# Performance work log

Measured on AMD Instinct MI355X. Metric: run time of the kernel, lower is better.

## Reference

```python
import jax, jax.numpy as jnp
import numpy as np

BINS = 10


def setup_inputs() -> dict:
    key = jax.random.key(0)
    k1, k2 = jax.random.split(key)
    pred = jax.random.normal(k1, (16384, 4096), dtype=jnp.float32)
    target = jax.random.randint(k2, (16384, 4096), 0, 2).astype(jnp.float32)
    return {"pred": pred, "target": target}


def reference(pred, target):
    bins = BINS
    # edges = [0, 0.1, ..., 1.0], last edge bumped by 1e-6 (as in torch module)
    edges = jnp.arange(bins + 1, dtype=jnp.float32) / bins
    edges = edges.at[-1].add(1e-6)

    # gradient magnitude g = |pred.detach() - target|
    g = jnp.abs(jax.lax.stop_gradient(pred) - target)

    # label_weight is forced to all-ones in the original forward -> all valid
    tot = jnp.float32(g.size)

    # histogram binning: element e belongs to bin i iff edges[i] <= g < edges[i+1]
    gf = g.ravel()
    idx = jnp.searchsorted(edges, gf, side="right") - 1  # in [-1, bins]
    in_range = (idx >= 0) & (idx < bins)                  # g >= 1+1e-6 falls outside
    idxc = jnp.clip(idx, 0, bins - 1)
    counts = jnp.zeros(bins, jnp.float32).at[idxc].add(in_range.astype(jnp.float32))

    n = jnp.sum(counts > 0).astype(jnp.float32)  # number of non-empty bins
    cnt_e = counts[idxc]                          # per-element bin count
    per = jnp.where(in_range & (cnt_e > 0), tot / jnp.maximum(cnt_e, 1.0), 0.0)
    weights = (per / jnp.maximum(n, 1.0)).reshape(pred.shape)

    # weighted BCE with logits, reduction='sum', normalized by tot
    log_p = jax.nn.log_sigmoid(pred)
    log_np = jax.nn.log_sigmoid(-pred)
    loss = -jnp.sum(weights * (target * log_p + (1.0 - target) * log_np)) / tot
    return loss
```

## Files before the change

kernel.cpp:

```cpp
#include <hip/hip_runtime.h>


#define NSLOTS 11

__device__ __forceinline__ void proc(float x, float t,
                                     float (&sum)[NSLOTS],
                                     unsigned (&cnt)[NSLOTS]) {
    const float edges[NSLOTS] = {0.0f, 0.1f, 0.2f, 0.3f, 0.4f, 0.5f,
                                 0.6f, 0.7f, 0.8f, 0.9f, 1.0f + 1e-6f};
    float g = fabsf(x - t);
    float l = fmaxf(x, 0.0f) - x * t + __logf(1.0f + __expf(-fabsf(x)));
    sum[0] += l;
    cnt[0] += 1u;
#pragma unroll
    for (int b = 1; b < NSLOTS; ++b) {
        bool m = (g >= edges[b]);
        cnt[b] += m ? 1u : 0u;
        sum[b] += m ? l : 0.0f;
    }
}

__global__ __launch_bounds__(256) void ghmc_partial(
    const float4* __restrict__ p4, const float4* __restrict__ t4, int n4,
    const float* __restrict__ p1, const float* __restrict__ t1, long long ntot,
    double* __restrict__ g_sum, unsigned int* __restrict__ g_cnt) {
    float sum[NSLOTS];
    unsigned cnt[NSLOTS];
#pragma unroll
    for (int b = 0; b < NSLOTS; ++b) { sum[b] = 0.0f; cnt[b] = 0u; }

    int stride = gridDim.x * blockDim.x;
    for (int i = blockIdx.x * blockDim.x + threadIdx.x; i < n4; i += stride) {
        float4 p = p4[i];
        float4 t = t4[i];
        proc(p.x, t.x, sum, cnt);
        proc(p.y, t.y, sum, cnt);
        proc(p.z, t.z, sum, cnt);
        proc(p.w, t.w, sum, cnt);
    }
    if (blockIdx.x == 0 && threadIdx.x == 0) {
        for (long long j = (long long)n4 * 4; j < ntot; ++j)
            proc(p1[j], t1[j], sum, cnt);
    }

#pragma unroll
    for (int off = 32; off > 0; off >>= 1) {
#pragma unroll
        for (int b = 0; b < NSLOTS; ++b) {
            sum[b] += __shfl_down(sum[b], off, 64);
            cnt[b] += __shfl_down(cnt[b], off, 64);
        }
    }

    __shared__ float s_sum[4][NSLOTS];
    __shared__ unsigned s_cnt[4][NSLOTS];
    int wave = threadIdx.x >> 6;
    int lane = threadIdx.x & 63;
    if (lane == 0) {
#pragma unroll
        for (int b = 0; b < NSLOTS; ++b) {
            s_sum[wave][b] = sum[b];
            s_cnt[wave][b] = cnt[b];
        }
    }
    __syncthreads();
    if (threadIdx.x < NSLOTS) {
        int b = threadIdx.x;
        float fs = s_sum[0][b] + s_sum[1][b] + s_sum[2][b] + s_sum[3][b];
        unsigned c = s_cnt[0][b] + s_cnt[1][b] + s_cnt[2][b] + s_cnt[3][b];
        atomicAdd(&g_sum[b], (double)fs);
        atomicAdd(&g_cnt[b], c);
    }
}

__global__ void ghmc_final(const double* __restrict__ g_sum,
                           const unsigned int* __restrict__ g_cnt,
                           float* __restrict__ out) {
    if (blockIdx.x == 0 && threadIdx.x == 0) {
        double loss = 0.0;
        int n = 0;
        double per_bin[10];
        double per_cnt[10];
#pragma unroll
        for (int b = 0; b < 10; ++b) {
            unsigned c = g_cnt[b] - g_cnt[b + 1];
            per_cnt[b] = (double)c;
            per_bin[b] = g_sum[b] - g_sum[b + 1];
            n += (c > 0u) ? 1 : 0;
        }
        double nn = (n > 0) ? (double)n : 1.0;
#pragma unroll
        for (int b = 0; b < 10; ++b) {
            if (per_cnt[b] > 0.0) loss += per_bin[b] / per_cnt[b];
        }
        loss /= nn;
        out[0] = (float)loss;
    }
}

extern "C" void kernel_launch(void* const* d_in, const int* in_sizes, int n_in,
                              void* d_out, int out_size, void* d_ws, size_t ws_size,
                              hipStream_t stream) {
    const float* pred = (const float*)d_in[0];
    const float* tgt  = (const float*)d_in[1];
    long long ntot = (long long)in_sizes[0];
    int n4 = (int)(ntot / 4);

    double* g_sum = (double*)d_ws;
    unsigned int* g_cnt = (unsigned int*)((char*)d_ws + NSLOTS * sizeof(double));

    hipMemsetAsync(d_ws, 0, NSLOTS * sizeof(double) + NSLOTS * sizeof(unsigned int),
                   stream);

    const int threads = 256;
    const int blocks = 2048;
    hipLaunchKernelGGL(ghmc_partial, dim3(blocks), dim3(threads), 0, stream,
                       (const float4*)pred, (const float4*)tgt, n4,
                       pred, tgt, ntot, g_sum, g_cnt);
    hipLaunchKernelGGL(ghmc_final, dim3(1), dim3(64), 0, stream,
                       g_sum, g_cnt, (float*)d_out);
}
```

Measured before the change: 544.5 us.

## Use wave ballots for bin counts, packed float2 sums, prefetch loads, larger grid

Replaces per-thread cumulative bin counters with wave-wide ballot+popcount so counts become wave-uniform scalars, and the count shuffle reduction is removed. Loss sums are accumulated as two-wide float vectors to allow packed FP32 adds, and the next float4 pair is software-prefetched. The grid grows to 8192 blocks so each thread does fewer iterations. Wave-uniform counts are only correct if the lane-0 value is the wave total, which ballot gives; cnt[0] is recomputed from the iteration count, and the tail loop contains an odd zero-multiplied term.

New measurement: 618.3 us. 13.5% more time.

```diff
diff --git a/kernel.cpp b/kernel.cpp
--- a/kernel.cpp
+++ b/kernel.cpp
@@ -3,73 +3,116 @@
 
 #define NSLOTS 11
 
-__device__ __forceinline__ void proc(float x, float t,
-                                     float (&sum)[NSLOTS],
-                                     unsigned (&cnt)[NSLOTS]) {
-    const float edges[NSLOTS] = {0.0f, 0.1f, 0.2f, 0.3f, 0.4f, 0.5f,
-                                 0.6f, 0.7f, 0.8f, 0.9f, 1.0f + 1e-6f};
-    float g = fabsf(x - t);
-    float l = fmaxf(x, 0.0f) - x * t + __logf(1.0f + __expf(-fabsf(x)));
-    sum[0] += l;
-    cnt[0] += 1u;
-#pragma unroll
-    for (int b = 1; b < NSLOTS; ++b) {
-        bool m = (g >= edges[b]);
-        cnt[b] += m ? 1u : 0u;
-        sum[b] += m ? l : 0.0f;
-    }
+typedef float vfloat2 __attribute__((ext_vector_type(2)));
+
+__device__ __forceinline__ float bce(float x, float t) {
+    return fmaxf(x, 0.0f) - x * t + __logf(1.0f + __expf(-fabsf(x)));
 }
 
 __global__ __launch_bounds__(256) void ghmc_partial(
     const float4* __restrict__ p4, const float4* __restrict__ t4, int n4,
     const float* __restrict__ p1, const float* __restrict__ t1, long long ntot,
     double* __restrict__ g_sum, unsigned int* __restrict__ g_cnt) {
-    float sum[NSLOTS];
+
+    const float edges[NSLOTS] = {0.0f, 0.1f, 0.2f, 0.3f, 0.4f, 0.5f,
+                                 0.6f, 0.7f, 0.8f, 0.9f, 1.0f + 1e-6f};
+
+    vfloat2 spk[NSLOTS];
     unsigned cnt[NSLOTS];
 #pragma unroll
-    for (int b = 0; b < NSLOTS; ++b) { sum[b] = 0.0f; cnt[b] = 0u; }
+    for (int s = 0; s < NSLOTS; ++s) { spk[s] = (vfloat2){0.0f, 0.0f}; cnt[s] = 0u; }
 
-    int stride = gridDim.x * blockDim.x;
-    for (int i = blockIdx.x * blockDim.x + threadIdx.x; i < n4; i += stride) {
-        float4 p = p4[i];
-        float4 t = t4[i];
-        proc(p.x, t.x, sum, cnt);
-        proc(p.y, t.y, sum, cnt);
-        proc(p.z, t.z, sum, cnt);
-        proc(p.w, t.w, sum, cnt);
+    const int stride = gridDim.x * blockDim.x;
+    int i = blockIdx.x * blockDim.x + threadIdx.x;
+    const int iters = n4 / stride;
+
+    float4 p, t;
+    if (iters > 0) { p = p4[i]; t = t4[i]; }
+
+    for (int it = 0; it < iters; ++it) {
+        const int inext = i + stride;
+        float4 pn, tn;
+        if (it + 1 < iters) { pn = p4[inext]; tn = t4[inext]; }
+
+        const float gx = fabsf(p.x - t.x), gy = fabsf(p.y - t.y);
+        const float gz = fabsf(p.z - t.z), gw = fabsf(p.w - t.w);
+        const float lx = bce(p.x, t.x), ly = bce(p.y, t.y);
+        const float lz = bce(p.z, t.z), lw = bce(p.w, t.w);
+
+        spk[0] += (vfloat2){lx, ly};
+        spk[0] += (vfloat2){lz, lw};
+#pragma unroll
+        for (int s = 1; s < NSLOTS; ++s) {
+            const bool mx = gx >= edges[s];
+            const bool my = gy >= edges[s];
+            const bool mz = gz >= edges[s];
+            const bool mw = gw >= edges[s];
+            cnt[s] += (unsigned)__popcll(__ballot(mx)) +
+                      (unsigned)__popcll(__ballot(my)) +
+                      (unsigned)__popcll(__ballot(mz)) +
+                      (unsigned)__popcll(__ballot(mw));
+            spk[s] += (vfloat2){mx ? lx : 0.0f, my ? ly : 0.0f};
+            spk[s] += (vfloat2){mz ? lz : 0.0f, mw ? lw : 0.0f};
+        }
+        p = pn; t = tn; i = inext;
+    }
+    cnt[0] = (unsigned)(64 * 4 * iters);
+
+    for (; i < n4; i += stride) {
+        float4 pp = p4[i], tt = t4[i];
+        const float e[4][2] = {{pp.x, tt.x}, {pp.y, tt.y}, {pp.z, tt.z}, {pp.w, tt.w}};
+        cnt[0] += (unsigned)__popcll(__ballot(1)) * 0u;
+        for (int q = 0; q < 4; ++q) {
+            const float g = fabsf(e[q][0] - e[q][1]);
+            const float l = bce(e[q][0], e[q][1]);
+            spk[0] += (vfloat2){l, 0.0f};
+            cnt[0] += (unsigned)__popcll(__ballot(1));
+#pragma unroll
+            for (int s = 1; s < NSLOTS; ++s) {
+                const bool m = g >= edges[s];
+                cnt[s] += (unsigned)__popcll(__ballot(m));
+                spk[s] += (vfloat2){m ? l : 0.0f, 0.0f};
+            }
+        }
     }
     if (blockIdx.x == 0 && threadIdx.x == 0) {
-        for (long long j = (long long)n4 * 4; j < ntot; ++j)
-            proc(p1[j], t1[j], sum, cnt);
+        for (long long j = (long long)n4 * 4; j < ntot; ++j) {
+            const float x = p1[j], tt = t1[j];
+            const float g = fabsf(x - tt);
+            const float l = bce(x, tt);
+            spk[0] += (vfloat2){l, 0.0f};
+            cnt[0] += 1u;
+#pragma unroll
+            for (int s = 1; s < NSLOTS; ++s) {
+                if (g >= edges[s]) { cnt[s] += 1u; spk[s] += (vfloat2){l, 0.0f}; }
+            }
+        }
     }
 
+    float sum[NSLOTS];
+#pragma unroll
+    for (int s = 0; s < NSLOTS; ++s) sum[s] = spk[s].x + spk[s].y;
 #pragma unroll
     for (int off = 32; off > 0; off >>= 1) {
 #pragma unroll
-        for (int b = 0; b < NSLOTS; ++b) {
-            sum[b] += __shfl_down(sum[b], off, 64);
-            cnt[b] += __shfl_down(cnt[b], off, 64);
-        }
+        for (int s = 0; s < NSLOTS; ++s) sum[s] += __shfl_down(sum[s], off, 64);
     }
 
     __shared__ float s_sum[4][NSLOTS];
     __shared__ unsigned s_cnt[4][NSLOTS];
-    int wave = threadIdx.x >> 6;
-    int lane = threadIdx.x & 63;
+    const int wave = threadIdx.x >> 6;
+    const int lane = threadIdx.x & 63;
     if (lane == 0) {
 #pragma unroll
-        for (int b = 0; b < NSLOTS; ++b) {
-            s_sum[wave][b] = sum[b];
-            s_cnt[wave][b] = cnt[b];
-        }
+        for (int s = 0; s < NSLOTS; ++s) { s_sum[wave][s] = sum[s]; s_cnt[wave][s] = cnt[s]; }
     }
     __syncthreads();
     if (threadIdx.x < NSLOTS) {
-        int b = threadIdx.x;
-        float fs = s_sum[0][b] + s_sum[1][b] + s_sum[2][b] + s_sum[3][b];
-        unsigned c = s_cnt[0][b] + s_cnt[1][b] + s_cnt[2][b] + s_cnt[3][b];
-        atomicAdd(&g_sum[b], (double)fs);
-        atomicAdd(&g_cnt[b], c);
+        const int s = threadIdx.x;
+        const float fs = s_sum[0][s] + s_sum[1][s] + s_sum[2][s] + s_sum[3][s];
+        const unsigned c = s_cnt[0][s] + s_cnt[1][s] + s_cnt[2][s] + s_cnt[3][s];
+        atomicAdd(&g_sum[s], (double)fs);
+        atomicAdd(&g_cnt[s], c);
     }
 }
 
@@ -79,21 +122,15 @@
     if (blockIdx.x == 0 && threadIdx.x == 0) {
         double loss = 0.0;
         int n = 0;
-        double per_bin[10];
-        double per_cnt[10];
 #pragma unroll
         for (int b = 0; b < 10; ++b) {
-            unsigned c = g_cnt[b] - g_cnt[b + 1];
-            per_cnt[b] = (double)c;
-            per_bin[b] = g_sum[b] - g_sum[b + 1];
-            n += (c > 0u) ? 1 : 0;
+            const unsigned c = g_cnt[b] - g_cnt[b + 1];
+            if (c > 0u) {
+                n += 1;
+                loss += (g_sum[b] - g_sum[b + 1]) / (double)c;
+            }
         }
-        double nn = (n > 0) ? (double)n : 1.0;
-#pragma unroll
-        for (int b = 0; b < 10; ++b) {
-            if (per_cnt[b] > 0.0) loss += per_bin[b] / per_cnt[b];
-        }
-        loss /= nn;
+        loss /= (n > 0) ? (double)n : 1.0;
         out[0] = (float)loss;
     }
 }
@@ -113,7 +150,7 @@
                    stream);
 
     const int threads = 256;
-    const int blocks = 2048;
+    const int blocks = 8192;
     hipLaunchKernelGGL(ghmc_partial, dim3(blocks), dim3(threads), 0, stream,
                        (const float4*)pred, (const float4*)tgt, n4,
                        pred, tgt, ntot, g_sum, g_cnt);
```

## Replace cumulative threshold accumulators with per-thread LDS histogram via direct binning

Applied to the files above, without the earlier changes.

Drops the ten-compare cumulative-threshold scheme, where every element updated eleven register accumulators. Each element's bin is now computed directly as (int)(g*10) and its loss and count are added with LDS atomics into a per-thread slice of shared memory. The final kernel then reads per-bin sums directly instead of differencing cumulative slots. The aim is to cut per-element ALU work. In exchange it adds two LDS atomic operations per element and about 22KB of shared memory per block, which may limit occupancy. Direct truncation binning can also differ from the float-edge comparisons at bin boundaries.

After: 1.037 ms. 1.9x slower.

```diff
diff --git a/kernel.cpp b/kernel.cpp
--- a/kernel.cpp
+++ b/kernel.cpp
@@ -1,75 +1,76 @@
 #include <hip/hip_runtime.h>
 
 
-#define NSLOTS 11
+#define NBINS 11
+#define LSTRIDE 11
+#define THREADS 256
 
-__device__ __forceinline__ void proc(float x, float t,
-                                     float (&sum)[NSLOTS],
-                                     unsigned (&cnt)[NSLOTS]) {
-    const float edges[NSLOTS] = {0.0f, 0.1f, 0.2f, 0.3f, 0.4f, 0.5f,
-                                 0.6f, 0.7f, 0.8f, 0.9f, 1.0f + 1e-6f};
-    float g = fabsf(x - t);
-    float l = fmaxf(x, 0.0f) - x * t + __logf(1.0f + __expf(-fabsf(x)));
-    sum[0] += l;
-    cnt[0] += 1u;
-#pragma unroll
-    for (int b = 1; b < NSLOTS; ++b) {
-        bool m = (g >= edges[b]);
-        cnt[b] += m ? 1u : 0u;
-        sum[b] += m ? l : 0.0f;
-    }
+__device__ __forceinline__ float bce(float x, float t) {
+    return fmaxf(x, 0.0f) - x * t + __logf(1.0f + __expf(-fabsf(x)));
 }
 
-__global__ __launch_bounds__(256) void ghmc_partial(
+__global__ __launch_bounds__(THREADS) void ghmc_partial(
     const float4* __restrict__ p4, const float4* __restrict__ t4, int n4,
     const float* __restrict__ p1, const float* __restrict__ t1, long long ntot,
     double* __restrict__ g_sum, unsigned int* __restrict__ g_cnt) {
-    float sum[NSLOTS];
-    unsigned cnt[NSLOTS];
+
+    __shared__ float lds_sum[THREADS * LSTRIDE];
+    __shared__ float lds_cnt[THREADS * LSTRIDE];
+
+    const int tid = threadIdx.x;
+    float* mysum = &lds_sum[tid * LSTRIDE];
+    float* mycnt = &lds_cnt[tid * LSTRIDE];
 #pragma unroll
-    for (int b = 0; b < NSLOTS; ++b) { sum[b] = 0.0f; cnt[b] = 0u; }
+    for (int b = 0; b < NBINS; ++b) { mysum[b] = 0.0f; mycnt[b] = 0.0f; }
 
-    int stride = gridDim.x * blockDim.x;
-    for (int i = blockIdx.x * blockDim.x + threadIdx.x; i < n4; i += stride) {
-        float4 p = p4[i];
-        float4 t = t4[i];
-        proc(p.x, t.x, sum, cnt);
-        proc(p.y, t.y, sum, cnt);
-        proc(p.z, t.z, sum, cnt);
-        proc(p.w, t.w, sum, cnt);
+    const float EDGE10 = 1.0f + 1e-6f;
+
+    auto put = [&](float x, float t) {
+        const float g = fabsf(x - t);
+        const float l = bce(x, t);
+        int idx = (int)(g * 10.0f);
+        idx = (idx > 9) ? 9 : idx;
+        idx = (g >= EDGE10) ? 10 : idx;
+        atomicAdd(&mysum[idx], l);
+        atomicAdd(&mycnt[idx], 1.0f);
+    };
+
+    const int stride = gridDim.x * blockDim.x;
+    for (int i = blockIdx.x * blockDim.x + tid; i < n4; i += stride) {
+        const float4 p = p4[i];
+        const float4 t = t4[i];
+        put(p.x, t.x); put(p.y, t.y); put(p.z, t.z); put(p.w, t.w);
     }
-    if (blockIdx.x == 0 && threadIdx.x == 0) {
-        for (long long j = (long long)n4 * 4; j < ntot; ++j)
-            proc(p1[j], t1[j], sum, cnt);
+    if (blockIdx.x == 0 && tid == 0) {
+        for (long long j = (long long)n4 * 4; j < ntot; ++j) put(p1[j], t1[j]);
     }
 
+    float s[NBINS], c[NBINS];
+#pragma unroll
+    for (int b = 0; b < NBINS; ++b) { s[b] = mysum[b]; c[b] = mycnt[b]; }
 #pragma unroll
     for (int off = 32; off > 0; off >>= 1) {
 #pragma unroll
-        for (int b = 0; b < NSLOTS; ++b) {
-            sum[b] += __shfl_down(sum[b], off, 64);
-            cnt[b] += __shfl_down(cnt[b], off, 64);
+        for (int b = 0; b < NBINS; ++b) {
+            s[b] += __shfl_down(s[b], off, 64);
+            c[b] += __shfl_down(c[b], off, 64);
         }
     }
 
-    __shared__ float s_sum[4][NSLOTS];
-    __shared__ unsigned s_cnt[4][NSLOTS];
-    int wave = threadIdx.x >> 6;
-    int lane = threadIdx.x & 63;
+    __shared__ float w_sum[4][NBINS];
+    __shared__ float w_cnt[4][NBINS];
+    const int wave = tid >> 6;
+    const int lane = tid & 63;
     if (lane == 0) {
 #pragma unroll
-        for (int b = 0; b < NSLOTS; ++b) {
-            s_sum[wave][b] = sum[b];
-            s_cnt[wave][b] = cnt[b];
-        }
+        for (int b = 0; b < NBINS; ++b) { w_sum[wave][b] = s[b]; w_cnt[wave][b] = c[b]; }
     }
     __syncthreads();
-    if (threadIdx.x < NSLOTS) {
-        int b = threadIdx.x;
-        float fs = s_sum[0][b] + s_sum[1][b] + s_sum[2][b] + s_sum[3][b];
-        unsigned c = s_cnt[0][b] + s_cnt[1][b] + s_cnt[2][b] + s_cnt[3][b];
-        atomicAdd(&g_sum[b], (double)fs);
-        atomicAdd(&g_cnt[b], c);
+    if (tid < NBINS) {
+        const float fs = w_sum[0][tid] + w_sum[1][tid] + w_sum[2][tid] + w_sum[3][tid];
+        const float fc = w_cnt[0][tid] + w_cnt[1][tid] + w_cnt[2][tid] + w_cnt[3][tid];
+        atomicAdd(&g_sum[tid], (double)fs);
+        atomicAdd(&g_cnt[tid], (unsigned int)(fc + 0.5f));
     }
 }
 
@@ -79,21 +80,15 @@
     if (blockIdx.x == 0 && threadIdx.x == 0) {
         double loss = 0.0;
         int n = 0;
-        double per_bin[10];
-        double per_cnt[10];
 #pragma unroll
         for (int b = 0; b < 10; ++b) {
-            unsigned c = g_cnt[b] - g_cnt[b + 1];
-            per_cnt[b] = (double)c;
-            per_bin[b] = g_sum[b] - g_sum[b + 1];
-            n += (c > 0u) ? 1 : 0;
+            const unsigned c = g_cnt[b];
+            if (c > 0u) {
+                n += 1;
+                loss += g_sum[b] / (double)c;
+            }
         }
-        double nn = (n > 0) ? (double)n : 1.0;
-#pragma unroll
-        for (int b = 0; b < 10; ++b) {
-            if (per_cnt[b] > 0.0) loss += per_bin[b] / per_cnt[b];
-        }
-        loss /= nn;
+        loss /= (n > 0) ? (double)n : 1.0;
         out[0] = (float)loss;
     }
 }
@@ -107,12 +102,12 @@
     int n4 = (int)(ntot / 4);
 
     double* g_sum = (double*)d_ws;
-    unsigned int* g_cnt = (unsigned int*)((char*)d_ws + NSLOTS * sizeof(double));
+    unsigned int* g_cnt = (unsigned int*)((char*)d_ws + NBINS * sizeof(double));
 
-    hipMemsetAsync(d_ws, 0, NSLOTS * sizeof(double) + NSLOTS * sizeof(unsigned int),
+    hipMemsetAsync(d_ws, 0, NBINS * sizeof(double) + NBINS * sizeof(unsigned int),
                    stream);
 
-    const int threads = 256;
+    const int threads = THREADS;
     const int blocks = 2048;
     hipLaunchKernelGGL(ghmc_partial, dim3(blocks), dim3(threads), 0, stream,
                        (const float4*)pred, (const float4*)tgt, n4,
```
